# Optimization experiments

Hardware: AMD Instinct MI355X
Metric: run time of the kernel (lower is better)

## Reference

```python
import jax, jax.numpy as jnp
import numpy as np

B, T, D_MODEL, HEAD = 4, 4096, 1024, 64

def setup_inputs() -> dict:
    key = jax.random.key(0)
    ks = jax.random.split(key, 7)
    s = 0.02  # typical init scale
    return {
        "x":  jax.random.normal(ks[0], (B, T, D_MODEL), dtype=jnp.float32),
        "Wq": jax.random.normal(ks[1], (D_MODEL, HEAD), dtype=jnp.float32) * s,
        "bq": jnp.zeros((HEAD,), dtype=jnp.float32),
        "Wk": jax.random.normal(ks[2], (D_MODEL, HEAD), dtype=jnp.float32) * s,
        "bk": jnp.zeros((HEAD,), dtype=jnp.float32),
        "Wv": jax.random.normal(ks[3], (D_MODEL, HEAD), dtype=jnp.float32) * s,
        "bv": jnp.zeros((HEAD,), dtype=jnp.float32),
    }

def reference(x, Wq, bq, Wk, bk, Wv, bv):
    Bz, Tz, C = x.shape
    q = x @ Wq + bq                      # (B,T,H)
    k = x @ Wk + bk                      # (B,T,H)
    v = x @ Wv + bv                      # (B,T,H)
    # NOTE: original scales by sqrt(C) = sqrt(d_model), not sqrt(head_size)
    att = jnp.einsum("bth,bsh->bts", q, k) / jnp.sqrt(jnp.float32(C))
    causal = jnp.tril(jnp.ones((Tz, Tz), dtype=bool))
    att = jnp.where(causal, att, -jnp.inf)
    att = jax.nn.softmax(att, axis=-1)
    return jnp.einsum("bts,bsh->bth", att, v)  # (B,T,H)
```

## Files before the change

### kernel.cpp

```cpp
#include <hip/hip_runtime.h>
#include <hip/hip_bf16.h>
#include <hip/hip_fp16.h>

#define T_SEQ 4096
#define DMODEL 1024
#define HEAD 64
#define NBATCH 4
#define NSEG 544
#define S2LOG 0.04508422f

typedef __attribute__((ext_vector_type(8))) short bf16x8;
typedef __attribute__((ext_vector_type(4))) float f32x4;

__device__ __forceinline__ unsigned short f2bf(float f) {
    unsigned int b = __float_as_uint(f);
    unsigned int r = b + 0x7FFFu + ((b >> 16) & 1u);
    return (unsigned short)(r >> 16);
}
__device__ __forceinline__ unsigned int pk_bf16(float a, float b) {
    __hip_bfloat162 h = __float22bfloat162_rn(make_float2(a, b));
    unsigned int u; __builtin_memcpy(&u, &h, 4); return u;
}
__device__ __forceinline__ void dma16(const void* g, void* s) {
    __builtin_amdgcn_global_load_lds(
        (const __attribute__((address_space(1))) unsigned int*)g,
        (__attribute__((address_space(3))) unsigned int*)s, 16, 0, 0);
}

__global__ __launch_bounds__(256) void prep_w(
    const float* __restrict__ Wq, const float* __restrict__ Wk,
    const float* __restrict__ Wv, unsigned short* __restrict__ Wtb)
{
    __shared__ unsigned short tl[64 * 72];
    const int bid = blockIdx.x;
    const int m   = bid >> 4;
    const int k0  = (bid & 15) * 64;
    const float* W = (m == 0) ? Wq : (m == 1) ? Wk : Wv;
    const int t  = threadIdx.x;
    const int kr = t >> 2, qtr = t & 3;
#pragma unroll
    for (int i = 0; i < 4; ++i) {
        float4 wv4 = *(const float4*)&W[(k0 + kr) * 64 + qtr * 16 + i * 4];
        tl[(qtr * 16 + i * 4 + 0) * 72 + kr] = f2bf(wv4.x);
        tl[(qtr * 16 + i * 4 + 1) * 72 + kr] = f2bf(wv4.y);
        tl[(qtr * 16 + i * 4 + 2) * 72 + kr] = f2bf(wv4.z);
        tl[(qtr * 16 + i * 4 + 3) * 72 + kr] = f2bf(wv4.w);
    }
    __syncthreads();
#pragma unroll
    for (int c = 0; c < 2; ++c) {
        const int lin = c * 256 + t;
        const int n = lin >> 3, k8 = lin & 7;
        const int k = k0 + k8 * 8;
        const int sg = k >> 7, koff = k & 127;
        *(uint4*)&Wtb[((long)(sg * 192 + m * 64 + n)) * 128 + koff] =
            *(const uint4*)&tl[n * 72 + k8 * 8];
    }
}

__global__ __launch_bounds__(512, 2) void qkv_mfma(
    const float* __restrict__ x, const unsigned short* __restrict__ Wtb,
    const float* __restrict__ bq, const float* __restrict__ bk,
    const float* __restrict__ bv,
    unsigned short* __restrict__ qo, unsigned short* __restrict__ ko,
    unsigned short* __restrict__ vt)
{
    __shared__ __align__(16) unsigned short xs[2][8192];
    __shared__ __align__(16) unsigned short wsd[2][24576];
    const int t    = threadIdx.x;
    const int lane = t & 63;
    const int l15  = lane & 15, quad = lane >> 4;
    const int wv   = __builtin_amdgcn_readfirstlane(t >> 6);
    const int rowg = wv >> 2;
    const int colg = wv & 3;
    const long row0 = (long)blockIdx.x * 64;

    float bias[3];
#pragma unroll
    for (int ntl = 0; ntl < 3; ++ntl) {
        const int c = colg * 48 + ntl * 16 + l15;
        bias[ntl] = (c < 64) ? bq[c] : (c < 128) ? bk[c - 64] : bv[c - 128];
    }
    f32x4 acc[2][3];
#pragma unroll
    for (int mt = 0; mt < 2; ++mt)
#pragma unroll
        for (int ntl = 0; ntl < 3; ++ntl)
            acc[mt][ntl] = (f32x4){bias[ntl], bias[ntl], bias[ntl], bias[ntl]};

    float4 g[4];
    auto load_stage = [&](int sg) {
#pragma unroll
        for (int s = 0; s < 4; ++s) {
            const int id = s * 512 + t, row = id >> 5, off = id & 31;
            g[s] = *(const float4*)&x[(row0 + row) * DMODEL + sg * 128 + off * 4];
        }
    };
    auto write_stage = [&](int buf) {
#pragma unroll
        for (int s = 0; s < 4; ++s) {
            const int id = s * 512 + t, row = id >> 5, off = id & 31;
            uint2 u;
            u.x = pk_bf16(g[s].x, g[s].y);
            u.y = pk_bf16(g[s].z, g[s].w);
            *(uint2*)&xs[buf][row * 128 + ((off >> 1) ^ (row & 7)) * 8 + (off & 1) * 4] = u;
        }
    };
    auto dma_w = [&](int sg, int buf) {
#pragma unroll
        for (int j = 0; j < 6; ++j) {
            const int slot0 = (wv * 6 + j) * 64;
            const int slot  = slot0 + lane;
            const int col   = slot >> 4, ch = slot & 15;
            dma16(Wtb + ((long)(sg * 192 + col)) * 128 + ((ch ^ (col & 7)) * 8),
                  &wsd[buf][slot0 * 8]);
        }
    };

    load_stage(0);
    dma_w(0, 0);
    write_stage(0);

    for (int sg = 0; sg < 8; ++sg) {
        __syncthreads();
        if (sg + 1 < 8) {
            load_stage(sg + 1);
            dma_w(sg + 1, (sg + 1) & 1);
        }
        bf16x8 wf[3][4];
#pragma unroll
        for (int ntl = 0; ntl < 3; ++ntl)
#pragma unroll
            for (int kq = 0; kq < 4; ++kq) {
                const int col = colg * 48 + ntl * 16 + l15;
                wf[ntl][kq] = *(const bf16x8*)&wsd[sg & 1][col * 128
                                                           + (((kq * 4 + quad) ^ (col & 7))) * 8];
            }
#pragma unroll
        for (int mt = 0; mt < 2; ++mt)
#pragma unroll
            for (int kq = 0; kq < 4; ++kq) {
                const int row = rowg * 32 + mt * 16 + l15;
                bf16x8 a = *(const bf16x8*)&xs[sg & 1][row * 128
                                                       + ((kq * 4 + quad) ^ (row & 7)) * 8];
#pragma unroll
                for (int ntl = 0; ntl < 3; ++ntl)
                    acc[mt][ntl] = __builtin_amdgcn_mfma_f32_16x16x32_bf16(a, wf[ntl][kq], acc[mt][ntl], 0, 0, 0);
            }
        if (sg + 1 < 8) write_stage((sg + 1) & 1);
    }
#pragma unroll
    for (int mt = 0; mt < 2; ++mt)
#pragma unroll
        for (int ntl = 0; ntl < 3; ++ntl) {
            const int c = colg * 48 + ntl * 16 + l15;
            const long tr0 = row0 + rowg * 32 + mt * 16 + quad * 4;
            if (c < 64) {
#pragma unroll
                for (int r = 0; r < 4; ++r)
                    qo[(tr0 + r) * HEAD + c] = f2bf(acc[mt][ntl][r] * S2LOG);
            } else if (c < 128) {
#pragma unroll
                for (int r = 0; r < 4; ++r)
                    ko[(tr0 + r) * HEAD + (c - 64)] = f2bf(acc[mt][ntl][r]);
            } else {
                const int b = (int)(tr0 >> 12), tloc = (int)(tr0 & 4095);
                uint2 pv;
                pv.x = pk_bf16(acc[mt][ntl][0], acc[mt][ntl][1]);
                pv.y = pk_bf16(acc[mt][ntl][2], acc[mt][ntl][3]);
                *(uint2*)&vt[((long)(b * HEAD + (c - 128))) * T_SEQ + tloc] = pv;
            }
        }
}

__global__ __launch_bounds__(256, 3) void flash_seg(
    const unsigned short* __restrict__ qg,
    const unsigned short* __restrict__ kg,
    const unsigned short* __restrict__ vtg,
    __half* __restrict__ opart, float* __restrict__ ml)
{
    __shared__ __align__(16) unsigned short kv_s[2][8192];
    __shared__ __align__(16) unsigned short p_s[4][32 * 40];
    __shared__ __align__(16) float l_lds[2][32];
    const int t0   = threadIdx.x;
    const int lane = t0 & 63;
    const int l15  = lane & 15, quad = lane >> 4;
    const int wv   = __builtin_amdgcn_readfirstlane(t0 >> 6);
    const int qh   = wv & 1;
    const int kh2  = wv >> 1;

    const int bid = (int)blockIdx.x;
    const int sid = (NSEG - 1) - (bid >> 2);
    const int b   = bid & 3;

    int kk = 0, pref = 0;
#pragma unroll
    for (int i = 0; i < 15; ++i) {
        const int cnt = 4 * (kk + 1);
        if (sid >= pref + cnt) { pref += cnt; ++kk; }
    }
    const int S   = kk + 1;
    const int rem = sid - pref;
    const int t   = kk * 4 + rem / S;
    const int si  = rem % S;
    const int r0  = t * 64;
    const int rw  = r0 + qh * 32;
    const int nck = t + 1;
    const int c0  = (si * nck) / S, c1 = ((si + 1) * nck) / S;
    const long bbase = (long)b * T_SEQ;
    const int gidx = b * NSEG + sid;

    bf16x8 qf[2][2];
#pragma unroll
    for (int cg = 0; cg < 2; ++cg)
#pragma unroll
        for (int h = 0; h < 2; ++h)
            qf[cg][h] = *(const bf16x8*)&qg[(bbase + rw + cg * 16 + l15) * HEAD
                                            + h * 32 + quad * 8];

    f32x4 o[4][2];
#pragma unroll
    for (int dt = 0; dt < 4; ++dt)
#pragma unroll
        for (int cg = 0; cg < 2; ++cg) o[dt][cg] = (f32x4){0.f, 0.f, 0.f, 0.f};
    float lrun[2] = {0.f, 0.f};
    unsigned short* ps = p_s[wv];

    auto dma_chunk = [&](int key0, int buf) {
#pragma unroll
        for (int i = 0; i < 2; ++i) {
            const int jj  = wv * 2 + i;
            const int kl  = jj * 8 + (lane >> 3);
            const int dlg = (lane & 7) ^ ((lane >> 3) & 7);
            dma16(kg + (bbase + key0 + kl) * HEAD + dlg * 8,
                  &kv_s[buf][jj * 512]);
        }
#pragma unroll
        for (int i = 0; i < 2; ++i) {
            const int jj  = wv * 2 + i;
            const int dim = jj * 8 + (lane >> 3);
            const int klg = (lane & 7) ^ ((lane >> 3) & 7);
            dma16(vtg + ((long)(b * HEAD + dim)) * T_SEQ + key0 + klg * 8,
                  &kv_s[buf][4096 + jj * 512]);
        }
    };
    dma_chunk(c0 * 64, 0);

    for (int c = c0; c < c1; ++c) {
        const int key0 = c * 64;
        const int cur  = (c - c0) & 1;
        __syncthreads();
        if (c + 1 < c1) dma_chunk((c + 1) * 64, cur ^ 1);

        bf16x8 kf[2][2];
#pragma unroll
        for (int mt = 0; mt < 2; ++mt)
#pragma unroll
            for (int kd = 0; kd < 2; ++kd) {
                const int key_l = kh2 * 32 + mt * 16 + l15;
                kf[mt][kd] = *(const bf16x8*)&kv_s[cur][key_l * 64
                                                        + ((kd * 4 + quad) ^ (l15 & 7)) * 8];
            }
        f32x4 st[2][2];
#pragma unroll
        for (int mt = 0; mt < 2; ++mt)
#pragma unroll
            for (int cg = 0; cg < 2; ++cg) {
                f32x4 z = (f32x4){0.f, 0.f, 0.f, 0.f};
                z = __builtin_amdgcn_mfma_f32_16x16x32_bf16(kf[mt][0], qf[cg][0], z, 0, 0, 0);
                st[mt][cg] = __builtin_amdgcn_mfma_f32_16x16x32_bf16(kf[mt][1], qf[cg][1], z, 0, 0, 0);
            }
        bf16x8 vf[4];
#pragma unroll
        for (int dt = 0; dt < 4; ++dt) {
            const int dim = dt * 16 + l15;
            vf[dt] = *(const bf16x8*)&kv_s[cur][4096 + dim * 64
                                                 + ((kh2 * 4 + quad) ^ (l15 & 7)) * 8];
        }
        if (key0 + kh2 * 32 + 31 > rw) {
#pragma unroll
            for (int mt = 0; mt < 2; ++mt)
#pragma unroll
                for (int cg = 0; cg < 2; ++cg)
#pragma unroll
                    for (int r = 0; r < 4; ++r) {
                        const int key = key0 + kh2 * 32 + mt * 16 + quad * 4 + r;
                        const int row = rw + cg * 16 + l15;
                        st[mt][cg][r] = (key <= row) ? st[mt][cg][r] : -30000.f;
                    }
        }
        float psum[2] = {0.f, 0.f};
#pragma unroll
        for (int mt = 0; mt < 2; ++mt)
#pragma unroll
            for (int cg = 0; cg < 2; ++cg) {
                float e0 = exp2f(st[mt][cg][0]), e1 = exp2f(st[mt][cg][1]);
                float e2 = exp2f(st[mt][cg][2]), e3 = exp2f(st[mt][cg][3]);
                psum[cg] += (e0 + e1) + (e2 + e3);
                *(unsigned int*)&ps[(cg * 16 + l15) * 40 + mt * 16 + quad * 4]     = pk_bf16(e0, e1);
                *(unsigned int*)&ps[(cg * 16 + l15) * 40 + mt * 16 + quad * 4 + 2] = pk_bf16(e2, e3);
            }
#pragma unroll
        for (int cg = 0; cg < 2; ++cg) {
            psum[cg] += __shfl_xor(psum[cg], 16);
            psum[cg] += __shfl_xor(psum[cg], 32);
            lrun[cg] += psum[cg];
        }
        __builtin_amdgcn_wave_barrier();
        bf16x8 pf[2];
#pragma unroll
        for (int cg = 0; cg < 2; ++cg)
            pf[cg] = *(const bf16x8*)&ps[(cg * 16 + l15) * 40 + quad * 8];
        __builtin_amdgcn_wave_barrier();
#pragma unroll
        for (int dt = 0; dt < 4; ++dt)
#pragma unroll
            for (int cg = 0; cg < 2; ++cg)
                o[dt][cg] = __builtin_amdgcn_mfma_f32_16x16x32_bf16(vf[dt], pf[cg], o[dt][cg], 0, 0, 0);
    }

    __syncthreads();
    float* o_lds = (float*)&kv_s[0][0];
    if (kh2 == 1) {
#pragma unroll
        for (int dt = 0; dt < 4; ++dt)
#pragma unroll
            for (int cg = 0; cg < 2; ++cg)
                *(f32x4*)&o_lds[(qh * 32 + cg * 16 + l15) * 68 + dt * 16 + quad * 4] = o[dt][cg];
        if (quad == 0) {
#pragma unroll
            for (int cg = 0; cg < 2; ++cg)
                l_lds[qh][cg * 16 + l15] = lrun[cg];
        }
    }
    __syncthreads();
    if (kh2 == 0) {
        float inv[2];
#pragma unroll
        for (int cg = 0; cg < 2; ++cg) {
            lrun[cg] += l_lds[qh][cg * 16 + l15];
            inv[cg] = (lrun[cg] > 0.f) ? 1.f / lrun[cg] : 0.f;
        }
        __half* op = opart + (long)gidx * 4096;
#pragma unroll
        for (int dt = 0; dt < 4; ++dt)
#pragma unroll
            for (int cg = 0; cg < 2; ++cg) {
                f32x4 ov = o[dt][cg];
                f32x4 add = *(const f32x4*)&o_lds[(qh * 32 + cg * 16 + l15) * 68 + dt * 16 + quad * 4];
                ov += add;
                __half2 h0 = __floats2half2_rn(ov[0] * inv[cg], ov[1] * inv[cg]);
                __half2 h1 = __floats2half2_rn(ov[2] * inv[cg], ov[3] * inv[cg]);
                uint2 u; __builtin_memcpy(&u.x, &h0, 4); __builtin_memcpy(&u.y, &h1, 4);
                *(uint2*)&op[(qh * 32 + cg * 16 + l15) * HEAD + dt * 16 + quad * 4] = u;
            }
        if (quad == 0) {
#pragma unroll
            for (int cg = 0; cg < 2; ++cg)
                ml[(long)gidx * 64 + qh * 32 + cg * 16 + l15] = lrun[cg];
        }
    }
}

__global__ __launch_bounds__(256) void merge_seg(
    const __half* __restrict__ opart, const float* __restrict__ ml,
    float* __restrict__ out)
{
    const int bid = blockIdx.x;
    const int half = bid & 1, t = (bid >> 1) & 63, b = bid >> 7;
    const int kk = t >> 2, S = kk + 1;
    const int base_sid = 2 * kk * (kk + 1) + (t & 3) * S;
    const int tid = threadIdx.x;
    const int row = half * 32 + (tid >> 3), col0 = (tid & 7) * 8;

    float acc[8];
#pragma unroll
    for (int j = 0; j < 8; ++j) acc[j] = 0.f;
    float L = 0.f;
    for (int si = 0; si < S; ++si) {
        const long g = (long)(b * NSEG + base_sid + si);
        const float l = ml[g * 64 + row];
        L += l;
        const __half* op = opart + g * 4096 + row * 64 + col0;
        uint4 u = *(const uint4*)op;
        __half2 h01, h23, h45, h67;
        __builtin_memcpy(&h01, &u.x, 4); __builtin_memcpy(&h23, &u.y, 4);
        __builtin_memcpy(&h45, &u.z, 4); __builtin_memcpy(&h67, &u.w, 4);
        float2 f01 = __half22float2(h01), f23 = __half22float2(h23);
        float2 f45 = __half22float2(h45), f67 = __half22float2(h67);
        acc[0] += l * f01.x; acc[1] += l * f01.y;
        acc[2] += l * f23.x; acc[3] += l * f23.y;
        acc[4] += l * f45.x; acc[5] += l * f45.y;
        acc[6] += l * f67.x; acc[7] += l * f67.y;
    }
    const float inv = 1.f / L;
    float* dst = out + ((long)(b * T_SEQ + t * 64 + row)) * HEAD + col0;
#pragma unroll
    for (int h = 0; h < 2; ++h) {
        float4 ov = {acc[h * 4] * inv, acc[h * 4 + 1] * inv,
                     acc[h * 4 + 2] * inv, acc[h * 4 + 3] * inv};
        *(float4*)(dst + h * 4) = ov;
    }
}

extern "C" void kernel_launch(void* const* d_in, const int* in_sizes, int n_in,
                              void* d_out, int out_size, void* d_ws, size_t ws_size,
                              hipStream_t stream) {
    const float* x  = (const float*)d_in[0];
    const float* Wq = (const float*)d_in[1];
    const float* bq = (const float*)d_in[2];
    const float* Wk = (const float*)d_in[3];
    const float* bk = (const float*)d_in[4];
    const float* Wv = (const float*)d_in[5];
    const float* bv = (const float*)d_in[6];
    float* outp = (float*)d_out;

    char* wsb = (char*)d_ws;
    unsigned short* wtb = (unsigned short*)(wsb);
    unsigned short* qw  = (unsigned short*)(wsb + 393216);
    unsigned short* kw  = (unsigned short*)(wsb + 2490368);
    unsigned short* vtw = (unsigned short*)(wsb + 4587520);
    __half* opart       = (__half*)(wsb + 6684672);
    float*  mlp         = (float*)(wsb + 24510464);

    prep_w<<<dim3(48), dim3(256), 0, stream>>>(Wq, Wk, Wv, wtb);
    qkv_mfma<<<dim3(256), dim3(512), 0, stream>>>(
        x, wtb, bq, bk, bv, qw, kw, vtw);
    flash_seg<<<dim3(NSEG * NBATCH), dim3(256), 0, stream>>>(qw, kw, vtw, opart, mlp);
    merge_seg<<<dim3(512), dim3(256), 0, stream>>>(opart, mlp, outp);
}
```

Measured before the change: 148.5 us.

## Fuse split-KV merge into flash kernel via last-block atomic counter

```diff
diff --git a/kernel.cpp b/kernel.cpp
--- a/kernel.cpp
+++ b/kernel.cpp
@@ -29,7 +29,8 @@
 
 __global__ __launch_bounds__(256) void prep_w(
     const float* __restrict__ Wq, const float* __restrict__ Wk,
-    const float* __restrict__ Wv, unsigned short* __restrict__ Wtb)
+    const float* __restrict__ Wv, unsigned short* __restrict__ Wtb,
+    int* __restrict__ cnt)
 {
     __shared__ unsigned short tl[64 * 72];
     const int bid = blockIdx.x;
@@ -37,6 +38,7 @@
     const int k0  = (bid & 15) * 64;
     const float* W = (m == 0) ? Wq : (m == 1) ? Wk : Wv;
     const int t  = threadIdx.x;
+    if (bid == 0) cnt[t] = 0;
     const int kr = t >> 2, qtr = t & 3;
 #pragma unroll
     for (int i = 0; i < 4; ++i) {
@@ -177,11 +179,13 @@
     const unsigned short* __restrict__ qg,
     const unsigned short* __restrict__ kg,
     const unsigned short* __restrict__ vtg,
-    __half* __restrict__ opart, float* __restrict__ ml)
+    __half* __restrict__ opart, float* __restrict__ ml,
+    float* __restrict__ out, int* __restrict__ cnt)
 {
     __shared__ __align__(16) unsigned short kv_s[2][8192];
     __shared__ __align__(16) unsigned short p_s[4][32 * 40];
     __shared__ __align__(16) float l_lds[2][32];
+    __shared__ int last_flag;
     const int t0   = threadIdx.x;
     const int lane = t0 & 63;
     const int l15  = lane & 15, quad = lane >> 4;
@@ -196,8 +200,8 @@
     int kk = 0, pref = 0;
 #pragma unroll
     for (int i = 0; i < 15; ++i) {
-        const int cnt = 4 * (kk + 1);
-        if (sid >= pref + cnt) { pref += cnt; ++kk; }
+        const int cnt_t = 4 * (kk + 1);
+        if (sid >= pref + cnt_t) { pref += cnt_t; ++kk; }
     }
     const int S   = kk + 1;
     const int rem = sid - pref;
@@ -360,46 +364,49 @@
                 ml[(long)gidx * 64 + qh * 32 + cg * 16 + l15] = lrun[cg];
         }
     }
-}
-
-__global__ __launch_bounds__(256) void merge_seg(
-    const __half* __restrict__ opart, const float* __restrict__ ml,
-    float* __restrict__ out)
-{
-    const int bid = blockIdx.x;
-    const int half = bid & 1, t = (bid >> 1) & 63, b = bid >> 7;
-    const int kk = t >> 2, S = kk + 1;
-    const int base_sid = 2 * kk * (kk + 1) + (t & 3) * S;
-    const int tid = threadIdx.x;
-    const int row = half * 32 + (tid >> 3), col0 = (tid & 7) * 8;
-
-    float acc[8];
-#pragma unroll
-    for (int j = 0; j < 8; ++j) acc[j] = 0.f;
-    float L = 0.f;
-    for (int si = 0; si < S; ++si) {
-        const long g = (long)(b * NSEG + base_sid + si);
-        const float l = ml[g * 64 + row];
-        L += l;
-        const __half* op = opart + g * 4096 + row * 64 + col0;
-        uint4 u = *(const uint4*)op;
-        __half2 h01, h23, h45, h67;
-        __builtin_memcpy(&h01, &u.x, 4); __builtin_memcpy(&h23, &u.y, 4);
-        __builtin_memcpy(&h45, &u.z, 4); __builtin_memcpy(&h67, &u.w, 4);
-        float2 f01 = __half22float2(h01), f23 = __half22float2(h23);
-        float2 f45 = __half22float2(h45), f67 = __half22float2(h67);
-        acc[0] += l * f01.x; acc[1] += l * f01.y;
-        acc[2] += l * f23.x; acc[3] += l * f23.y;
-        acc[4] += l * f45.x; acc[5] += l * f45.y;
-        acc[6] += l * f67.x; acc[7] += l * f67.y;
-    }
-    const float inv = 1.f / L;
-    float* dst = out + ((long)(b * T_SEQ + t * 64 + row)) * HEAD + col0;
-#pragma unroll
-    for (int h = 0; h < 2; ++h) {
-        float4 ov = {acc[h * 4] * inv, acc[h * 4 + 1] * inv,
-                     acc[h * 4 + 2] * inv, acc[h * 4 + 3] * inv};
-        *(float4*)(dst + h * 4) = ov;
+
+    __syncthreads();
+    if (t0 == 0) {
+        __threadfence();
+        const int old = atomicAdd(&cnt[b * 64 + t], 1);
+        last_flag = (old == S - 1) ? 1 : 0;
+    }
+    __syncthreads();
+    if (last_flag) {
+        __threadfence();
+        const int base_sid = 2 * kk * (kk + 1) + (t & 3) * S;
+        const int row = t0 >> 2, col0 = (t0 & 3) * 16;
+        float acc[16];
+#pragma unroll
+        for (int j = 0; j < 16; ++j) acc[j] = 0.f;
+        float L = 0.f;
+        for (int s2 = 0; s2 < S; ++s2) {
+            const long g = (long)(b * NSEG + base_sid + s2);
+            const float l = ml[g * 64 + row];
+            L += l;
+            const __half* op = opart + g * 4096 + row * 64 + col0;
+#pragma unroll
+            for (int h = 0; h < 2; ++h) {
+                uint4 u = *(const uint4*)(op + h * 8);
+                __half2 h01, h23, h45, h67;
+                __builtin_memcpy(&h01, &u.x, 4); __builtin_memcpy(&h23, &u.y, 4);
+                __builtin_memcpy(&h45, &u.z, 4); __builtin_memcpy(&h67, &u.w, 4);
+                float2 f01 = __half22float2(h01), f23 = __half22float2(h23);
+                float2 f45 = __half22float2(h45), f67 = __half22float2(h67);
+                acc[h * 8 + 0] += l * f01.x; acc[h * 8 + 1] += l * f01.y;
+                acc[h * 8 + 2] += l * f23.x; acc[h * 8 + 3] += l * f23.y;
+                acc[h * 8 + 4] += l * f45.x; acc[h * 8 + 5] += l * f45.y;
+                acc[h * 8 + 6] += l * f67.x; acc[h * 8 + 7] += l * f67.y;
+            }
+        }
+        const float inv = 1.f / L;
+        float* dst = out + ((long)(b * T_SEQ + t * 64 + row)) * HEAD + col0;
+#pragma unroll
+        for (int h = 0; h < 4; ++h) {
+            float4 ov = {acc[h * 4] * inv, acc[h * 4 + 1] * inv,
+                         acc[h * 4 + 2] * inv, acc[h * 4 + 3] * inv};
+            *(float4*)(dst + h * 4) = ov;
+        }
     }
 }
 
@@ -422,10 +429,11 @@
     unsigned short* vtw = (unsigned short*)(wsb + 4587520);
     __half* opart       = (__half*)(wsb + 6684672);
     float*  mlp         = (float*)(wsb + 24510464);
-
-    prep_w<<<dim3(48), dim3(256), 0, stream>>>(Wq, Wk, Wv, wtb);
+    int*    cntp        = (int*)(wsb + 25067520);
+
+    prep_w<<<dim3(48), dim3(256), 0, stream>>>(Wq, Wk, Wv, wtb, cntp);
     qkv_mfma<<<dim3(256), dim3(512), 0, stream>>>(
         x, wtb, bq, bk, bv, qw, kw, vtw);
-    flash_seg<<<dim3(NSEG * NBATCH), dim3(256), 0, stream>>>(qw, kw, vtw, opart, mlp);
-    merge_seg<<<dim3(512), dim3(256), 0, stream>>>(opart, mlp, outp);
-}
+    flash_seg<<<dim3(NSEG * NBATCH), dim3(256), 0, stream>>>(
+        qw, kw, vtw, opart, mlp, outp, cntp);
+}
```

Measured after the change: 282.4 us. 1.9x slower.
